# Optimization experiments

Measured on AMD Instinct MI355X. Metric: run time of the kernel, lower is better.

The kernel has to match this reference:

```python
import math
import jax, jax.numpy as jnp
import numpy as np

# ---- module hyperparameters (from init_kwargs) ----
MAX_DISP = 48
IMG_WIDTH = 1248
W = IMG_WIDTH // 4          # 312 rows of the OT problem (left pixels)
C_COLS = MAX_DISP + W       # 360 columns (shifted right pixels)
NUM_ITER = 10
TAU = 0.95
EPS = 1.0
KAPPA = (1.0 - TAU) / 2.0
XI = (1.0 - TAU) / (1.0 + TAU)
RHO = EPS * TAU / (1.0 - TAU)
BIG_COST = 10000.0

B, H = 2, 64


def setup_inputs() -> dict:
    key = jax.random.key(0)
    scores = jax.random.normal(key, (B, MAX_DISP, H, W), dtype=jnp.float32)
    return {"scores": scores}


def _masked(x):
    # torch.where(isfinite(x), x, 0)
    return jnp.where(jnp.isfinite(x), x, jnp.zeros_like(x))


def _lse_kernel(Cm, f, g, axis):
    # S = (C - f[...,None] - g[...,None,:]) / eps ; eps*logsumexp(-S, axis)
    S = (Cm - f[..., None] - g[..., None, :]) / EPS
    w_res = EPS * jax.nn.logsumexp(-S, axis=axis)
    w_sgn = f if axis == -1 else g
    return w_res - _masked(w_sgn)


def _sinkhorn_update(Cm, f, g, axis, log_marginal):
    app = _lse_kernel(Cm, f, g, axis)
    return EPS * log_marginal - _masked(app)


def _smin(h, log_marginal):
    return -RHO * jax.nn.logsumexp(-h / RHO + log_marginal, axis=-1)


def _unbalanced_ot(Cm):
    # Cm: (B,H,W,C_COLS) cost matrix
    log_a = jnp.full((W,), -math.log(W), dtype=Cm.dtype)
    log_b = jnp.full((C_COLS,), -math.log(C_COLS), dtype=Cm.dtype)

    f = -EPS * jax.nn.logsumexp(-Cm / EPS + log_b, axis=-1)          # (B,H,W)
    g = jnp.zeros(Cm.shape[:2] + (C_COLS,), dtype=Cm.dtype)          # (B,H,C)

    for _ in range(NUM_ITER):
        old_f = f
        new_g = TAU * _sinkhorn_update(Cm, old_f, g, axis=-2, log_marginal=log_b)
        new_g = new_g - KAPPA * _smin(old_f, log_a)[..., None]
        new_g = new_g + XI * _smin(new_g, log_b)[..., None]
        new_f = TAU * _sinkhorn_update(Cm, f, new_g, axis=-1, log_marginal=log_a)
        new_f = new_f - KAPPA * _smin(new_g, log_b)[..., None]
        new_f = new_f + XI * _smin(new_f, log_a)[..., None]
        f, g = new_f, new_g

    S = (Cm - f[..., None] - g[..., None, :]) / EPS
    return jnp.exp(-S)                                               # transport plan P


def _scatter_to_cost(scores):
    # (B,D,H,W) scores -> (B,H,W,C_COLS) cost, vectorized scatter over d
    Bn, D, Hn, Wn = scores.shape
    j = jnp.arange(Wn)
    d = jnp.arange(D)
    col = j[None, :] - d[:, None] + MAX_DISP                          # (D,W), all in-range, no collisions
    jj = jnp.broadcast_to(j[None, :], (D, Wn))
    cost = jnp.full((Bn, Hn, Wn, C_COLS), BIG_COST, dtype=scores.dtype)
    # scores (B,D,H,W) -> (B,H,D,W) to match fancy-index result shape
    cost = cost.at[:, :, jj, col].set(-jnp.transpose(scores, (0, 2, 1, 3)))
    return cost


def _plan_to_disparity(P, D):
    right = jnp.arange(C_COLS, dtype=P.dtype) - D
    left = jnp.arange(W, dtype=P.dtype)
    disp_map = left[:, None] - right[None, :]                         # (W,C)
    mass = jnp.clip(jnp.sum(P, axis=-1), 1e-8, None)                  # (B,H,W)
    disp = jnp.sum(P * disp_map, axis=-1) / mass                      # (B,H,W)
    return disp[:, None, :, :]                                        # (B,1,H,W)


def reference(scores):
    D = scores.shape[1]
    Cm = _scatter_to_cost(scores)
    P = _unbalanced_ot(Cm)
    return _plan_to_disparity(P, D)
```

## Files before the change

### kernel.cpp

```cpp
#include <hip/hip_runtime.h>
#include <math.h>


#define MAXD   48
#define WROWS  312
#define CCOLS  360
#define NITER  10
#define NT     768
#define KD     24
#define NACC   (2 * NITER + 1)

__device__ __forceinline__ float pair_sum(float x) {
    int y = __builtin_amdgcn_update_dpp(0, __float_as_int(x), 0xB1, 0xf, 0xf, true);
    return x + __int_as_float(y);
}
template <int CTRL>
__device__ __forceinline__ float dpp_add(float x, float acc) {
    int y = __builtin_amdgcn_update_dpp(0, __float_as_int(x), CTRL, 0xf, 0xf, true);
    return acc + __int_as_float(y);
}
__device__ __forceinline__ float dpp_sum64(float x) {
    x = dpp_add<0x111>(x, x);
    x = dpp_add<0x112>(x, x);
    x = dpp_add<0x114>(x, x);
    x = dpp_add<0x118>(x, x);
    x = dpp_add<0x142>(x, x);
    x = dpp_add<0x143>(x, x);
    return x;
}

__global__ __launch_bounds__(NT)
void ot_disp_kernel(const float* __restrict__ scores, float* __restrict__ out) {
    const int bid  = blockIdx.x;
    const int tid  = threadIdx.x;
    const int half = tid >> 1;
    const int sub  = tid & 1;

    const float LOG_A2 = -8.2854022f;
    const float LOG_B2 = -8.4918531f;
    const float TAU    = 0.95f;
    const float KAPPA  = 0.025f;
    const float XI     = 0.025641026f;
    const float RHO    = 19.0f;
    const float INVRHO = 0.052631579f;
    const float TIR    = 0.05f;

    __shared__ float2 sEA[204], sEB[205], sGA[180], sGB[181];
    __shared__ float  s_acc[NACC];
    float* const EAf = (float*)sEA;  float* const EBf = (float*)sEB;
    float* const GAf = (float*)sGA;  float* const GBf = (float*)sGB;

    if (tid < 205) {
        sEB[tid] = make_float2(0.f, 0.f);
        if (tid < 204) sEA[tid] = make_float2(0.f, 0.f);
        if (tid < 181) sGB[tid] = make_float2(0.f, 0.f);
        if (tid < 180) sGA[tid] = make_float2(0.f, 0.f);
    }
    if (tid < NACC) s_acc[tid] = 0.f;

    const bool rowAct = (half < WROWS);
    const bool colAct = (half >= 1 && half < CCOLS);
    const int b = bid >> 6, h = bid & 63;
    const float* src = scores + ((size_t)(b * MAXD) * 64 + h) * WROWS;
    const size_t dstr = (size_t)64 * WROWS;
    const int d0 = sub * KD;
    const int jr = rowAct ? half : 0;
    const int jc = colAct ? half : 0;

    float wcol[KD];
    float wrowR[KD];
    #pragma unroll
    for (int m = 0; m < KD; ++m) {
        wrowR[m] = __expf(src[dstr * (size_t)(d0 + 23 - m) + jr]);
        int j = jc - MAXD + d0 + m;
        bool v = colAct && ((unsigned)j < (unsigned)WROWS);
        float sv = src[dstr * (size_t)(d0 + m) + (v ? j : 0)];
        wcol[m] = v ? __expf(sv) : 0.0f;
    }

    const int pe = jc + d0;
    const float2* const ep = (pe & 1) ? (sEB + ((pe + 1) >> 1)) : (sEA + (pe >> 1));
    const int qg = jr + 25 - d0;
    const float2* const gp = (qg & 1) ? (sGB + ((qg + 1) >> 1)) : (sGA + (qg >> 1));

    __syncthreads();

    {
        float a0=0,a1=0,a2=0,a3=0;
        #pragma unroll
        for (int m = 0; m < KD; m += 4) {
            a0 += wrowR[m];   a1 += wrowR[m+1];
            a2 += wrowR[m+2]; a3 += wrowR[m+3];
        }
        float s  = pair_sum((a0 + a1) + (a2 + a3));
        float ls = __builtin_amdgcn_logf(s);
        float eh = __builtin_amdgcn_exp2f(-ls);
        bool own = rowAct && (sub == 0);
        if (own) { EAf[half + MAXD] = eh; EBf[half + MAXD + 1] = eh; }
        float yv = __builtin_amdgcn_exp2f(fmaf(INVRHO, ls, LOG_A2));
        float t  = dpp_sum64(own ? yv : 0.0f);
        if ((tid & 63) == 63) atomicAdd(&s_acc[0], t);
        __syncthreads();
    }

    float2 gv[12];
    float ehat = 0.f, den = 0.f;
    for (int it = 0; it < NITER; ++it) {
        float a0=0,a1=0,a2=0,a3=0;
        #pragma unroll
        for (int u = 0; u < 12; u += 2) {
            float2 v0 = ep[u], v1 = ep[u+1];
            a0 = fmaf(wcol[2*u],   v0.x, a0);
            a1 = fmaf(wcol[2*u+1], v0.y, a1);
            a2 = fmaf(wcol[2*u+2], v1.x, a2);
            a3 = fmaf(wcol[2*u+3], v1.y, a3);
        }
        float cs  = pair_sum((a0 + a1) + (a2 + a3));
        float lcs = __builtin_amdgcn_logf(cs);
        float gh  = __builtin_amdgcn_exp2f(-TAU * lcs);
        bool ownC = colAct && (sub == 0);
        if (ownC) { GAf[half] = gh; GBf[half + 1] = gh; }
        float yv = __builtin_amdgcn_exp2f(fmaf(TIR, lcs, LOG_B2));
        float tg = dpp_sum64(ownC ? yv : 0.0f);
        if ((tid & 63) == 63) atomicAdd(&s_acc[1 + 2*it], tg);
        __syncthreads();

        float b0=0,b1=0,b2=0,b3=0;
        #pragma unroll
        for (int u = 0; u < 12; u += 2) {
            gv[u] = gp[u]; gv[u+1] = gp[u+1];
            b0 = fmaf(wrowR[2*u],   gv[u].x,   b0);
            b1 = fmaf(wrowR[2*u+1], gv[u].y,   b1);
            b2 = fmaf(wrowR[2*u+2], gv[u+1].x, b2);
            b3 = fmaf(wrowR[2*u+3], gv[u+1].y, b3);
        }
        den = pair_sum((b0 + b1) + (b2 + b3));
        float lrs = __builtin_amdgcn_logf(den);
        ehat = __builtin_amdgcn_exp2f(-TAU * lrs);
        bool ownR = rowAct && (sub == 0);
        if (ownR) { EAf[half + MAXD] = ehat; EBf[half + MAXD + 1] = ehat; }
        float yf = __builtin_amdgcn_exp2f(fmaf(TIR, lrs, LOG_A2));
        float tf = dpp_sum64(ownR ? yf : 0.0f);
        if ((tid & 63) == 63) atomicAdd(&s_acc[2 + 2*it], tf);
        __syncthreads();
    }

    float R[NACC];
    #pragma unroll
    for (int t = 0; t < NACC; ++t) R[t] = __builtin_amdgcn_logf(s_acc[t]);
    float fsh   = -LOG_B2;
    float sminF = fsh - RHO * R[0];
    float gsh   = 0.f;
    #pragma unroll
    for (int it = 0; it < NITER; ++it) {
        float Cg = TAU * (LOG_B2 - fsh) - KAPPA * sminF;
        float sg = Cg - RHO * R[1 + 2*it];
        gsh = Cg + XI * sg;
        float sminG = (1.0f + XI) * sg;
        float Cf = TAU * (LOG_A2 - gsh) - KAPPA * sminG;
        float sf = Cf - RHO * R[2 + 2*it];
        fsh   = Cf + XI * sf;
        sminF = (1.0f + XI) * sf;
    }

    float n0 = 0.f, n1 = 0.f;
    #pragma unroll
    for (int u = 0; u < 12; ++u) {
        n0 = fmaf((float)(d0 + 23 - 2*u) * wrowR[2*u],   gv[u].x, n0);
        n1 = fmaf((float)(d0 + 22 - 2*u) * wrowR[2*u+1], gv[u].y, n1);
    }
    float num = pair_sum(n0 + n1);
    if (rowAct && sub == 0) {
        float E = __builtin_amdgcn_exp2f(fsh + gsh) * ehat;
        float mass = fmaxf(E * den, 1e-8f);
        out[(size_t)bid * WROWS + half] = (E * num) / mass;
    }
}

extern "C" void kernel_launch(void* const* d_in, const int* in_sizes, int n_in,
                              void* d_out, int out_size, void* d_ws, size_t ws_size,
                              hipStream_t stream) {
    const float* scores = (const float*)d_in[0];
    float* out = (float*)d_out;
    ot_disp_kernel<<<128, NT, 0, stream>>>(scores, out);
}
```

Baseline: 25.98 us.

## Rewrite OT kernel as single-wave blocks with fp16 packed dot products

Each block now runs one 64-lane wavefront instead of 768 threads. Every lane owns 6 rows and 6 columns, and the exp-scores are stored as packed fp16 so the matvecs use v_dot2 instructions. Scores are staged through an fp16 LDS tile, and the per-iteration partial sums are reduced once at the end with DPP instead of LDS atomics. This is meant to cut barrier and atomic overhead, at the cost of fp16 precision in the scaling vectors and much less parallelism per block, which means heavy per-lane serial work and high register pressure.

```diff
diff --git a/kernel.cpp b/kernel.cpp
--- a/kernel.cpp
+++ b/kernel.cpp
@@ -1,19 +1,29 @@
 #include <hip/hip_runtime.h>
 #include <math.h>
 
+
+typedef _Float16 half1;
+typedef _Float16 half2v __attribute__((ext_vector_type(2)));
 
 #define MAXD   48
 #define WROWS  312
 #define CCOLS  360
 #define NITER  10
-#define NT     768
-#define KD     24
-#define NACC   (2 * NITER + 1)
-
-__device__ __forceinline__ float pair_sum(float x) {
-    int y = __builtin_amdgcn_update_dpp(0, __float_as_int(x), 0xB1, 0xf, 0xf, true);
-    return x + __int_as_float(y);
-}
+#define NACC   21
+
+__device__ __forceinline__ half2v h2(unsigned v) { return __builtin_bit_cast(half2v, v); }
+__device__ __forceinline__ half2v pack2(unsigned short a, unsigned short b) {
+    unsigned u = (unsigned)a | ((unsigned)b << 16);
+    return __builtin_bit_cast(half2v, u);
+}
+__device__ __forceinline__ unsigned packf(float x, float y) {
+    half2v v; v[0] = (half1)x; v[1] = (half1)y;
+    return __builtin_bit_cast(unsigned, v);
+}
+__device__ __forceinline__ unsigned short f16b(float x) {
+    half1 v = (half1)x; return __builtin_bit_cast(unsigned short, v);
+}
+
 template <int CTRL>
 __device__ __forceinline__ float dpp_add(float x, float acc) {
     int y = __builtin_amdgcn_update_dpp(0, __float_as_int(x), CTRL, 0xf, 0xf, true);
@@ -29,125 +39,179 @@
     return x;
 }
 
-__global__ __launch_bounds__(NT)
+__global__ __launch_bounds__(64, 1)
 void ot_disp_kernel(const float* __restrict__ scores, float* __restrict__ out) {
-    const int bid  = blockIdx.x;
-    const int tid  = threadIdx.x;
-    const int half = tid >> 1;
-    const int sub  = tid & 1;
+    const int L   = threadIdx.x;
+    const int bid = blockIdx.x;
+    const int b   = bid >> 6, h = bid & 63;
 
     const float LOG_A2 = -8.2854022f;
     const float LOG_B2 = -8.4918531f;
-    const float TAU    = 0.95f;
-    const float KAPPA  = 0.025f;
-    const float XI     = 0.025641026f;
-    const float RHO    = 19.0f;
-    const float INVRHO = 0.052631579f;
-    const float TIR    = 0.05f;
-
-    __shared__ float2 sEA[204], sEB[205], sGA[180], sGB[181];
-    __shared__ float  s_acc[NACC];
-    float* const EAf = (float*)sEA;  float* const EBf = (float*)sEB;
-    float* const GAf = (float*)sGA;  float* const GBf = (float*)sGB;
-
-    if (tid < 205) {
-        sEB[tid] = make_float2(0.f, 0.f);
-        if (tid < 204) sEA[tid] = make_float2(0.f, 0.f);
-        if (tid < 181) sGB[tid] = make_float2(0.f, 0.f);
-        if (tid < 180) sGA[tid] = make_float2(0.f, 0.f);
-    }
-    if (tid < NACC) s_acc[tid] = 0.f;
-
-    const bool rowAct = (half < WROWS);
-    const bool colAct = (half >= 1 && half < CCOLS);
-    const int b = bid >> 6, h = bid & 63;
+    const float TAU = 0.95f, KAPPA = 0.025f, XI = 0.025641026f;
+    const float RHO = 19.0f, INVRHO = 0.052631579f, TIR = 0.05f;
+
+    __shared__ half1    wS[MAXD * WROWS];
+    __shared__ unsigned EA2[204];
+    __shared__ unsigned EB2[205];
+    __shared__ unsigned GA2[181];
+    __shared__ unsigned GB2[182];
+    __shared__ float    s_y[NACC * 64];
+
     const float* src = scores + ((size_t)(b * MAXD) * 64 + h) * WROWS;
     const size_t dstr = (size_t)64 * WROWS;
-    const int d0 = sub * KD;
-    const int jr = rowAct ? half : 0;
-    const int jc = colAct ? half : 0;
-
-    float wcol[KD];
-    float wrowR[KD];
-    #pragma unroll
-    for (int m = 0; m < KD; ++m) {
-        wrowR[m] = __expf(src[dstr * (size_t)(d0 + 23 - m) + jr]);
-        int j = jc - MAXD + d0 + m;
-        bool v = colAct && ((unsigned)j < (unsigned)WROWS);
-        float sv = src[dstr * (size_t)(d0 + m) + (v ? j : 0)];
-        wcol[m] = v ? __expf(sv) : 0.0f;
-    }
-
-    const int pe = jc + d0;
-    const float2* const ep = (pe & 1) ? (sEB + ((pe + 1) >> 1)) : (sEA + (pe >> 1));
-    const int qg = jr + 25 - d0;
-    const float2* const gp = (qg & 1) ? (sGB + ((qg + 1) >> 1)) : (sGA + (qg >> 1));
-
+
+    for (int d = 0; d < MAXD; ++d) {
+        #pragma unroll
+        for (int q = 0; q < 5; ++q) {
+            int j = 64 * q + L;
+            if (j < WROWS) wS[d * WROWS + j] = (half1)__expf(src[d * dstr + j]);
+        }
+    }
+    #pragma unroll
+    for (int k = 0; k < 4; ++k) {
+        int i = 64 * k + L;
+        if (i < 204) EA2[i] = 0u;
+        if (i < 205) EB2[i] = 0u;
+    }
+    #pragma unroll
+    for (int k = 0; k < 3; ++k) {
+        int i = 64 * k + L;
+        if (i < 181) GA2[i] = 0u;
+        if (i < 182) GB2[i] = 0u;
+    }
     __syncthreads();
 
+    const unsigned short* wSu = (const unsigned short*)wS;
+    const bool colLane = (L < 60);
+    const bool rowLane = (L < 52);
+    half2v wcolH[6][24];
+    half2v wrowH[6][24];
+    #pragma unroll
+    for (int m = 0; m < 6; ++m) {
+        #pragma unroll
+        for (int t = 0; t < 24; ++t) {
+            int c = 6 * L + m;
+            int j0 = c - MAXD + 2 * t, j1 = j0 + 1;
+            unsigned short a  = (colLane && (unsigned)j0 < (unsigned)WROWS) ? wSu[(2*t)*WROWS + j0]   : (unsigned short)0;
+            unsigned short bb = (colLane && (unsigned)j1 < (unsigned)WROWS) ? wSu[(2*t+1)*WROWS + j1] : (unsigned short)0;
+            wcolH[m][t] = pack2(a, bb);
+        }
+    }
+    #pragma unroll
+    for (int r = 0; r < 6; ++r) {
+        int j = 6 * L + r;
+        #pragma unroll
+        for (int t = 0; t < 24; ++t) {
+            unsigned short a  = rowLane ? wSu[(47 - 2*t)*WROWS + j] : (unsigned short)0;
+            unsigned short bb = rowLane ? wSu[(46 - 2*t)*WROWS + j] : (unsigned short)0;
+            wrowH[r][t] = pack2(a, bb);
+        }
+    }
+
+    const unsigned ONE2 = 0x3C003C00u;
     {
-        float a0=0,a1=0,a2=0,a3=0;
-        #pragma unroll
-        for (int m = 0; m < KD; m += 4) {
-            a0 += wrowR[m];   a1 += wrowR[m+1];
-            a2 += wrowR[m+2]; a3 += wrowR[m+3];
-        }
-        float s  = pair_sum((a0 + a1) + (a2 + a3));
-        float ls = __builtin_amdgcn_logf(s);
-        float eh = __builtin_amdgcn_exp2f(-ls);
-        bool own = rowAct && (sub == 0);
-        if (own) { EAf[half + MAXD] = eh; EBf[half + MAXD + 1] = eh; }
-        float yv = __builtin_amdgcn_exp2f(fmaf(INVRHO, ls, LOG_A2));
-        float t  = dpp_sum64(own ? yv : 0.0f);
-        if ((tid & 63) == 63) atomicAdd(&s_acc[0], t);
+        float y0 = 0.f, eh[6];
+        #pragma unroll
+        for (int r = 0; r < 6; ++r) {
+            float s = 0.f;
+            #pragma unroll
+            for (int t = 0; t < 24; ++t)
+                s = __builtin_amdgcn_fdot2(wrowH[r][t], h2(ONE2), s, false);
+            float l = __builtin_amdgcn_logf(s);
+            eh[r] = __builtin_amdgcn_exp2f(-l);
+            y0 += __builtin_amdgcn_exp2f(fmaf(INVRHO, l, LOG_A2));
+        }
+        if (rowLane) {
+            EA2[3*L + 24 + 0] = packf(eh[0], eh[1]);
+            EA2[3*L + 24 + 1] = packf(eh[2], eh[3]);
+            EA2[3*L + 24 + 2] = packf(eh[4], eh[5]);
+            unsigned short* EBu = (unsigned short*)EB2;
+            #pragma unroll
+            for (int r = 0; r < 6; ++r) EBu[6*L + 49 + r] = f16b(eh[r]);
+        }
+        s_y[L] = y0;
+    }
+    __syncthreads();
+
+    const int ebase = 3 * (colLane ? L : 59);
+    const int gbase = 3 * (rowLane ? L : 51);
+    float denv[6], ehv[6];
+
+    for (int it = 0; it < NITER; ++it) {
+        unsigned eA[27], eB[27];
+        #pragma unroll
+        for (int t = 0; t < 27; ++t) { eA[t] = EA2[ebase + t]; eB[t] = EB2[ebase + t]; }
+        float yc = 0.f, gh[6];
+        #pragma unroll
+        for (int m = 0; m < 6; ++m) {
+            float acc = 0.f;
+            const int off = (m + 1) >> 1;
+            if (m & 1) {
+                #pragma unroll
+                for (int t = 0; t < 24; ++t)
+                    acc = __builtin_amdgcn_fdot2(wcolH[m][t], h2(eB[off + t]), acc, false);
+            } else {
+                #pragma unroll
+                for (int t = 0; t < 24; ++t)
+                    acc = __builtin_amdgcn_fdot2(wcolH[m][t], h2(eA[off + t]), acc, false);
+            }
+            float lc = __builtin_amdgcn_logf(acc);
+            gh[m] = __builtin_amdgcn_exp2f(-TAU * lc);
+            yc += __builtin_amdgcn_exp2f(fmaf(TIR, lc, LOG_B2));
+        }
+        if (colLane) {
+            GA2[3*L + 0] = packf(gh[0], gh[1]);
+            GA2[3*L + 1] = packf(gh[2], gh[3]);
+            GA2[3*L + 2] = packf(gh[4], gh[5]);
+            unsigned short* GBu = (unsigned short*)GB2;
+            #pragma unroll
+            for (int m = 0; m < 6; ++m) GBu[6*L + 1 + m] = f16b(gh[m]);
+        }
+        s_y[(1 + 2*it) * 64 + L] = yc;
         __syncthreads();
-    }
-
-    float2 gv[12];
-    float ehat = 0.f, den = 0.f;
-    for (int it = 0; it < NITER; ++it) {
-        float a0=0,a1=0,a2=0,a3=0;
-        #pragma unroll
-        for (int u = 0; u < 12; u += 2) {
-            float2 v0 = ep[u], v1 = ep[u+1];
-            a0 = fmaf(wcol[2*u],   v0.x, a0);
-            a1 = fmaf(wcol[2*u+1], v0.y, a1);
-            a2 = fmaf(wcol[2*u+2], v1.x, a2);
-            a3 = fmaf(wcol[2*u+3], v1.y, a3);
-        }
-        float cs  = pair_sum((a0 + a1) + (a2 + a3));
-        float lcs = __builtin_amdgcn_logf(cs);
-        float gh  = __builtin_amdgcn_exp2f(-TAU * lcs);
-        bool ownC = colAct && (sub == 0);
-        if (ownC) { GAf[half] = gh; GBf[half + 1] = gh; }
-        float yv = __builtin_amdgcn_exp2f(fmaf(TIR, lcs, LOG_B2));
-        float tg = dpp_sum64(ownC ? yv : 0.0f);
-        if ((tid & 63) == 63) atomicAdd(&s_acc[1 + 2*it], tg);
+
+        unsigned gA[27], gB[27];
+        #pragma unroll
+        for (int t = 0; t < 27; ++t) { gA[t] = GA2[gbase + t]; gB[t] = GB2[gbase + t]; }
+        float yr = 0.f;
+        #pragma unroll
+        for (int r = 0; r < 6; ++r) {
+            float acc = 0.f;
+            const int off = (r >> 1) + 1;
+            if (r & 1) {
+                #pragma unroll
+                for (int t = 0; t < 24; ++t)
+                    acc = __builtin_amdgcn_fdot2(wrowH[r][t], h2(gA[off + t]), acc, false);
+            } else {
+                #pragma unroll
+                for (int t = 0; t < 24; ++t)
+                    acc = __builtin_amdgcn_fdot2(wrowH[r][t], h2(gB[off + t]), acc, false);
+            }
+            denv[r] = acc;
+            float lr = __builtin_amdgcn_logf(acc);
+            ehv[r] = __builtin_amdgcn_exp2f(-TAU * lr);
+            yr += __builtin_amdgcn_exp2f(fmaf(TIR, lr, LOG_A2));
+        }
+        if (rowLane) {
+            EA2[3*L + 24 + 0] = packf(ehv[0], ehv[1]);
+            EA2[3*L + 24 + 1] = packf(ehv[2], ehv[3]);
+            EA2[3*L + 24 + 2] = packf(ehv[4], ehv[5]);
+            unsigned short* EBu = (unsigned short*)EB2;
+            #pragma unroll
+            for (int r = 0; r < 6; ++r) EBu[6*L + 49 + r] = f16b(ehv[r]);
+        }
+        s_y[(2 + 2*it) * 64 + L] = yr;
         __syncthreads();
-
-        float b0=0,b1=0,b2=0,b3=0;
-        #pragma unroll
-        for (int u = 0; u < 12; u += 2) {
-            gv[u] = gp[u]; gv[u+1] = gp[u+1];
-            b0 = fmaf(wrowR[2*u],   gv[u].x,   b0);
-            b1 = fmaf(wrowR[2*u+1], gv[u].y,   b1);
-            b2 = fmaf(wrowR[2*u+2], gv[u+1].x, b2);
-            b3 = fmaf(wrowR[2*u+3], gv[u+1].y, b3);
-        }
-        den = pair_sum((b0 + b1) + (b2 + b3));
-        float lrs = __builtin_amdgcn_logf(den);
-        ehat = __builtin_amdgcn_exp2f(-TAU * lrs);
-        bool ownR = rowAct && (sub == 0);
-        if (ownR) { EAf[half + MAXD] = ehat; EBf[half + MAXD + 1] = ehat; }
-        float yf = __builtin_amdgcn_exp2f(fmaf(TIR, lrs, LOG_A2));
-        float tf = dpp_sum64(ownR ? yf : 0.0f);
-        if ((tid & 63) == 63) atomicAdd(&s_acc[2 + 2*it], tf);
-        __syncthreads();
     }
 
     float R[NACC];
     #pragma unroll
-    for (int t = 0; t < NACC; ++t) R[t] = __builtin_amdgcn_logf(s_acc[t]);
+    for (int p = 0; p < NACC; ++p) {
+        float s = dpp_sum64(s_y[p * 64 + L]);
+        s = __shfl(s, 63);
+        R[p] = __builtin_amdgcn_logf(s);
+    }
+
     float fsh   = -LOG_B2;
     float sminF = fsh - RHO * R[0];
     float gsh   = 0.f;
@@ -156,24 +220,33 @@
         float Cg = TAU * (LOG_B2 - fsh) - KAPPA * sminF;
         float sg = Cg - RHO * R[1 + 2*it];
         gsh = Cg + XI * sg;
-        float sminG = (1.0f + XI) * sg;
+        float sminG = (1.f + XI) * sg;
         float Cf = TAU * (LOG_A2 - gsh) - KAPPA * sminG;
         float sf = Cf - RHO * R[2 + 2*it];
-        fsh   = Cf + XI * sf;
-        sminF = (1.0f + XI) * sf;
-    }
-
-    float n0 = 0.f, n1 = 0.f;
-    #pragma unroll
-    for (int u = 0; u < 12; ++u) {
-        n0 = fmaf((float)(d0 + 23 - 2*u) * wrowR[2*u],   gv[u].x, n0);
-        n1 = fmaf((float)(d0 + 22 - 2*u) * wrowR[2*u+1], gv[u].y, n1);
-    }
-    float num = pair_sum(n0 + n1);
-    if (rowAct && sub == 0) {
-        float E = __builtin_amdgcn_exp2f(fsh + gsh) * ehat;
-        float mass = fmaxf(E * den, 1e-8f);
-        out[(size_t)bid * WROWS + half] = (E * num) / mass;
+        fsh = Cf + XI * sf;
+        sminF = (1.f + XI) * sf;
+    }
+
+    if (rowLane) {
+        unsigned gAe[27], gBe[27];
+        #pragma unroll
+        for (int t = 0; t < 27; ++t) { gAe[t] = GA2[gbase + t]; gBe[t] = GB2[gbase + t]; }
+        float escale = __builtin_amdgcn_exp2f(fsh + gsh);
+        #pragma unroll
+        for (int r = 0; r < 6; ++r) {
+            float num = 0.f;
+            const int off = (r >> 1) + 1;
+            #pragma unroll
+            for (int t = 0; t < 24; ++t) {
+                half2v dc; dc[0] = (half1)(float)(47 - 2*t); dc[1] = (half1)(float)(46 - 2*t);
+                half2v wd = wrowH[r][t] * dc;
+                unsigned gp = (r & 1) ? gAe[off + t] : gBe[off + t];
+                num = __builtin_amdgcn_fdot2(wd, h2(gp), num, false);
+            }
+            float E = escale * ehv[r];
+            float mass = fmaxf(E * denv[r], 1e-8f);
+            out[(size_t)bid * WROWS + 6*L + r] = (E * num) / mass;
+        }
     }
 }
 
@@ -182,5 +255,5 @@
                               hipStream_t stream) {
     const float* scores = (const float*)d_in[0];
     float* out = (float*)d_out;
-    ot_disp_kernel<<<128, NT, 0, stream>>>(scores, out);
-}
+    ot_disp_kernel<<<128, 64, 0, stream>>>(scores, out);
+}
```

Result: slower. 72.98 us (+180.9%).
